# Optimization experiments

Measured on AMD Instinct MI355X. Metric: run time of the kernel, lower is better.

Reference implementation:

```python
import jax, jax.numpy as jnp
import numpy as np

RMS_EPS = 1e-6
B, S, H = 2, 4096, 4096
N_Q_OUT, N_KV_OUT = 4096, 1024  # 32 heads * 128, 8 kv heads * 128


def setup_inputs() -> dict:
    key = jax.random.key(0)
    k1, k2, k3, k4 = jax.random.split(key, 4)
    scale = 1.0 / np.sqrt(H)
    return {
        "hidden_states": jax.random.normal(k1, (B, S, H), dtype=jnp.float32),
        "gamma": jnp.ones((H,), dtype=jnp.float32),
        "w_q": jax.random.normal(k2, (H, N_Q_OUT), dtype=jnp.float32) * scale,
        "w_k": jax.random.normal(k3, (H, N_KV_OUT), dtype=jnp.float32) * scale,
        "w_v": jax.random.normal(k4, (H, N_KV_OUT), dtype=jnp.float32) * scale,
    }


def _rmsnorm(x, gamma, eps=RMS_EPS):
    # x: [B, S, H]; normalize over last axis
    var = jnp.mean(jnp.square(x), axis=-1, keepdims=True)
    return x * jax.lax.rsqrt(var + eps) * gamma


def reference(hidden_states, gamma, w_q, w_k, w_v):
    # Fused RMSNorm + QKV projection (GQA): normalize once, then three
    # column-parallel matmuls sharing the normalized activation.
    xn = _rmsnorm(hidden_states, gamma)  # [B, S, H]
    q = jnp.einsum("bsh,hd->bsd", xn, w_q)  # [B, S, n_heads*head_dim]
    k = jnp.einsum("bsh,hd->bsd", xn, w_k)  # [B, S, n_kv_heads*head_dim]
    v = jnp.einsum("bsh,hd->bsd", xn, w_v)  # [B, S, n_kv_heads*head_dim]
    return q, k, v
```

## Files before the change

### kernel.cpp

```cpp
#include <hip/hip_runtime.h>
#include <hip/hip_bf16.h>
#include <stdint.h>

#define HD      4096
#define MROWS   8192
#define NQ      4096
#define NKV     1024
#define NTOT    6144
#define RMS_EPS 1e-6f

typedef __attribute__((ext_vector_type(8))) short bf16x8;
typedef __attribute__((ext_vector_type(16))) float f32x16;

static __device__ __forceinline__ unsigned short f2bf(float f) {
  union { float f; unsigned u; } a; a.f = f;
  unsigned r = a.u + 0x7FFFu + ((a.u >> 16) & 1u);
  return (unsigned short)(r >> 16);
}

__global__ __launch_bounds__(256) void rmsnorm_cast_kernel(
    const float* __restrict__ x, const float* __restrict__ gamma,
    unsigned short* __restrict__ xn) {
  const int row = blockIdx.x;
  const float4* xr = (const float4*)(x + (size_t)row * HD);
  const float4* g4 = (const float4*)gamma;
  const int t = threadIdx.x;
  float4 v[4];
  float ss = 0.f;
#pragma unroll
  for (int i = 0; i < 4; ++i) {
    v[i] = xr[t + i * 256];
    ss += v[i].x * v[i].x + v[i].y * v[i].y + v[i].z * v[i].z + v[i].w * v[i].w;
  }
#pragma unroll
  for (int o = 32; o > 0; o >>= 1) ss += __shfl_xor(ss, o, 64);
  __shared__ float red[4];
  if ((t & 63) == 0) red[t >> 6] = ss;
  __syncthreads();
  const float tot = red[0] + red[1] + red[2] + red[3];
  const float rstd = rsqrtf(tot * (1.f / HD) + RMS_EPS);
  ushort4* xo = (ushort4*)(xn + (size_t)row * HD);
#pragma unroll
  for (int i = 0; i < 4; ++i) {
    const float4 g = g4[t + i * 256];
    ushort4 o;
    o.x = f2bf(v[i].x * rstd * g.x);
    o.y = f2bf(v[i].y * rstd * g.y);
    o.z = f2bf(v[i].z * rstd * g.z);
    o.w = f2bf(v[i].w * rstd * g.w);
    xo[t + i * 256] = o;
  }
}

__global__ __launch_bounds__(256) void transpose_cast_kernel(
    const float* __restrict__ w, unsigned short* __restrict__ wt, int Nw) {
  __shared__ float tile[32][33];
  const int kt = blockIdx.y;
  const int nb = blockIdx.x;
  const int t = threadIdx.x;
  const int r = t >> 3, c4 = t & 7;
  const float4 vin = *(const float4*)&w[(size_t)(kt * 32 + r) * Nw + nb * 32 + c4 * 4];
  tile[r][c4 * 4 + 0] = vin.x;
  tile[r][c4 * 4 + 1] = vin.y;
  tile[r][c4 * 4 + 2] = vin.z;
  tile[r][c4 * 4 + 3] = vin.w;
  __syncthreads();
  ushort4 o;
  o.x = f2bf(tile[c4 * 4 + 0][r]);
  o.y = f2bf(tile[c4 * 4 + 1][r]);
  o.z = f2bf(tile[c4 * 4 + 2][r]);
  o.w = f2bf(tile[c4 * 4 + 3][r]);
  *(ushort4*)&wt[(size_t)(nb * 32 + r) * HD + kt * 32 + c4 * 4] = o;
}


static __device__ __forceinline__ void gload_lds16(const unsigned short* g,
                                                   unsigned short* l) {
  __builtin_amdgcn_global_load_lds(
      (const __attribute__((address_space(1))) void*)g,
      (__attribute__((address_space(3))) void*)l, 16, 0, 0);
}

#define VM4 asm volatile("s_waitcnt vmcnt(4)" ::: "memory")
#define VM0 asm volatile("s_waitcnt vmcnt(0)" ::: "memory")

#define RD_A(BUF, HA)                                                          \
  do {                                                                         \
    const char* Ah = (const char*)&lds[0][BUF][HA][0];                         \
    _Pragma("unroll") for (int mi = 0; mi < 2; ++mi)                           \
      _Pragma("unroll") for (int ks = 0; ks < 4; ++ks)                         \
        af[mi][ks] = *(const bf16x8*)(Ah + (wr * 64 + mi * 32 + r32) * 128 +   \
                                      (((ks * 2 + hi) ^ swx) << 4));           \
  } while (0)

#define RD_B(BUF, HB)                                                          \
  do {                                                                         \
    const char* Bh = (const char*)&lds[1][BUF][HB][0];                         \
    _Pragma("unroll") for (int ks = 0; ks < 4; ++ks)                           \
      bfr[ks] = *(const bf16x8*)(Bh + (wc * 32 + r32) * 128 +                  \
                                 (((ks * 2 + hi) ^ swx) << 4));                \
  } while (0)

#define MMA(HA, HB)                                                            \
  do {                                                                         \
    __builtin_amdgcn_s_barrier();                                              \
    __builtin_amdgcn_s_setprio(1);                                             \
    _Pragma("unroll") for (int ks = 0; ks < 4; ++ks)                           \
      _Pragma("unroll") for (int mi = 0; mi < 2; ++mi)                         \
        acc[(HA) * 2 + mi][HB] = __builtin_amdgcn_mfma_f32_32x32x16_bf16(      \
            af[mi][ks], bfr[ks], acc[(HA) * 2 + mi][HB], 0, 0, 0);             \
    __builtin_amdgcn_s_setprio(0);                                             \
  } while (0)

__global__ __launch_bounds__(512, 2) void gemm_qkv_kernel(
    const unsigned short* __restrict__ A,
    const unsigned short* __restrict__ Bt,
    float* __restrict__ out) {
  __shared__ unsigned short lds[2][2][2][8192] __attribute__((aligned(16)));

  const int bid = blockIdx.x;
  const int xcd = bid & 7;
  const int idx = bid >> 3;
  const int sr  = idx >> 5;
  const int i32 = idx & 31;
  const int mt  = (xcd >> 1) * 8 + (i32 >> 2);
  const int nt  = (xcd & 1) * 12 + sr * 4 + (i32 & 3);
  const int m0 = mt * 256, n0 = nt * 256;

  const int tid = threadIdx.x;
  const int w = tid >> 6, lane = tid & 63;
  const int wr = w >> 2, wc = w & 3;
  const int r32 = lane & 31, hi = lane >> 5;
  const int swx = (r32 >> 1) & 7;

  const int wslot = w * 512;
  const int r3 = tid >> 3;
  const int scolb = (((tid & 7) ^ ((r3 >> 1) & 7))) << 4;
  const size_t so0 = (size_t)r3 * HD + (scolb >> 1);
  const size_t so1 = so0 + (size_t)64 * HD;

  const unsigned short* const Ab0 = A + (size_t)m0 * HD;
  const unsigned short* const Ab1 = Ab0 + (size_t)128 * HD;
  const unsigned short* const Bb0 = Bt + (size_t)n0 * HD;
  const unsigned short* const Bb1 = Bb0 + (size_t)128 * HD;

  auto STG = [&](const unsigned short* g, unsigned short* l) {
    gload_lds16(g + so0, l + wslot);
    gload_lds16(g + so1, l + 4096 + wslot);
  };

  f32x16 acc[4][2];
#pragma unroll
  for (int i = 0; i < 4; ++i)
#pragma unroll
    for (int j = 0; j < 2; ++j) acc[i][j] = (f32x16)(0.f);

  bf16x8 af[2][4];
  bf16x8 bfr[4];

  STG(Ab0, &lds[0][0][0][0]);
  STG(Bb0, &lds[1][0][0][0]);
  STG(Ab1, &lds[0][0][1][0]);
  STG(Bb1, &lds[1][0][1][0]);
  STG(Ab0 + 64, &lds[0][1][0][0]);
  STG(Bb0 + 64, &lds[1][1][0][0]);
  VM4;
  __builtin_amdgcn_s_barrier();

  for (int t = 0; t < 31; ++t) {
    const size_t k1 = (size_t)(2 * t + 1) * 64;
    const size_t o2 = (size_t)(2 * t + 2) * 64;
    const size_t o3 = (size_t)(2 * t + 3) * 64;
    RD_A(0, 0); RD_B(0, 1); STG(Ab1 + k1, &lds[0][1][1][0]);      MMA(0, 1);
    RD_B(0, 0);             STG(Bb1 + k1, &lds[1][1][1][0]);      MMA(0, 0);
    RD_A(0, 1);             STG(Ab0 + o2, &lds[0][0][0][0]);      MMA(1, 0);
    RD_B(0, 1);             STG(Bb0 + o2, &lds[1][0][0][0]); VM4; MMA(1, 1);
    RD_A(1, 0); RD_B(1, 1); STG(Ab1 + o2, &lds[0][0][1][0]);      MMA(0, 1);
    RD_B(1, 0);             STG(Bb1 + o2, &lds[1][0][1][0]);      MMA(0, 0);
    RD_A(1, 1);             STG(Ab0 + o3, &lds[0][1][0][0]);      MMA(1, 0);
    RD_B(1, 1);             STG(Bb0 + o3, &lds[1][1][0][0]); VM4; MMA(1, 1);
  }
  {
    const size_t k1 = (size_t)63 * 64;
    RD_A(0, 0); RD_B(0, 1); STG(Ab1 + k1, &lds[0][1][1][0]);      MMA(0, 1);
    RD_B(0, 0);             STG(Bb1 + k1, &lds[1][1][1][0]);      MMA(0, 0);
    RD_A(0, 1);                                                   MMA(1, 0);
    RD_B(0, 1);                                              VM0; MMA(1, 1);
    RD_A(1, 0); RD_B(1, 1);                                       MMA(0, 1);
    RD_B(1, 0);                                                   MMA(0, 0);
    RD_A(1, 1);                                                   MMA(1, 0);
    RD_B(1, 1);                                                   MMA(1, 1);
  }

  size_t obase; int ldc, nc;
  if (n0 < NQ)            { obase = 0;                                        ldc = NQ;  nc = n0; }
  else if (n0 < NQ + NKV) { obase = (size_t)MROWS * NQ;                       ldc = NKV; nc = n0 - NQ; }
  else                    { obase = (size_t)MROWS * NQ + (size_t)MROWS * NKV; ldc = NKV; nc = n0 - NQ - NKV; }

#pragma unroll
  for (int I = 0; I < 4; ++I) {
    const int rbase = m0 + (I >> 1) * 128 + wr * 64 + (I & 1) * 32 + hi * 4;
#pragma unroll
    for (int J = 0; J < 2; ++J) {
      const int col = nc + J * 128 + wc * 32 + r32;
#pragma unroll
      for (int reg = 0; reg < 16; ++reg) {
        const int row = rbase + (reg & 3) + 8 * (reg >> 2);
        out[obase + (size_t)row * ldc + col] = acc[I][J][reg];
      }
    }
  }
}

extern "C" void kernel_launch(void* const* d_in, const int* in_sizes, int n_in,
                              void* d_out, int out_size, void* d_ws, size_t ws_size,
                              hipStream_t stream) {
  const float* x     = (const float*)d_in[0];
  const float* gamma = (const float*)d_in[1];
  const float* wq    = (const float*)d_in[2];
  const float* wk    = (const float*)d_in[3];
  const float* wv    = (const float*)d_in[4];
  float* out = (float*)d_out;

  unsigned short* xn = (unsigned short*)d_ws;
  unsigned short* wt = xn + (size_t)MROWS * HD;

  rmsnorm_cast_kernel<<<MROWS, 256, 0, stream>>>(x, gamma, xn);
  transpose_cast_kernel<<<dim3(NQ / 32, HD / 32), 256, 0, stream>>>(wq, wt, NQ);
  transpose_cast_kernel<<<dim3(NKV / 32, HD / 32), 256, 0, stream>>>(
      wk, wt + (size_t)NQ * HD, NKV);
  transpose_cast_kernel<<<dim3(NKV / 32, HD / 32), 256, 0, stream>>>(
      wv, wt + (size_t)(NQ + NKV) * HD, NKV);
  gemm_qkv_kernel<<<(MROWS / 256) * (NTOT / 256), 512, 0, stream>>>(xn, wt, out);
}
```

Baseline: 416.0 us.

## Software-pipeline LDS fragment reads across MFMA halves with split K-subtiles

Splits each 64-wide K fragment into two halves with separate register sets, so LDS reads for the next MFMA group are issued while the current half's MFMAs run. Barriers move to after the MFMAs, and the global-to-LDS staging order is reshuffled with one extra prologue load and a deeper vmcnt wait. The goal is to hide LDS read latency behind matrix-core work. In exchange it needs more careful hazard ordering and may raise register pressure.

```diff
diff --git a/kernel.cpp b/kernel.cpp
--- a/kernel.cpp
+++ b/kernel.cpp
@@ -82,33 +82,57 @@
 }
 
 #define VM4 asm volatile("s_waitcnt vmcnt(4)" ::: "memory")
+#define VM6 asm volatile("s_waitcnt vmcnt(6)" ::: "memory")
 #define VM0 asm volatile("s_waitcnt vmcnt(0)" ::: "memory")
-
-#define RD_A(BUF, HA)                                                          \
+#define BAR __builtin_amdgcn_s_barrier()
+
+#define RA0(BUF, HA)                                                           \
   do {                                                                         \
     const char* Ah = (const char*)&lds[0][BUF][HA][0];                         \
     _Pragma("unroll") for (int mi = 0; mi < 2; ++mi)                           \
-      _Pragma("unroll") for (int ks = 0; ks < 4; ++ks)                         \
-        af[mi][ks] = *(const bf16x8*)(Ah + (wr * 64 + mi * 32 + r32) * 128 +   \
-                                      (((ks * 2 + hi) ^ swx) << 4));           \
-  } while (0)
-
-#define RD_B(BUF, HB)                                                          \
+      _Pragma("unroll") for (int k = 0; k < 2; ++k)                            \
+        af0[mi][k] = *(const bf16x8*)(Ah + (wr * 64 + mi * 32 + r32) * 128 +   \
+                                      (((k * 2 + hi) ^ swx) << 4));            \
+  } while (0)
+#define RA1(BUF, HA)                                                           \
+  do {                                                                         \
+    const char* Ah = (const char*)&lds[0][BUF][HA][0];                         \
+    _Pragma("unroll") for (int mi = 0; mi < 2; ++mi)                           \
+      _Pragma("unroll") for (int k = 0; k < 2; ++k)                            \
+        af1[mi][k] = *(const bf16x8*)(Ah + (wr * 64 + mi * 32 + r32) * 128 +   \
+                                      ((((k + 2) * 2 + hi) ^ swx) << 4));      \
+  } while (0)
+#define RB0(BUF, HB)                                                           \
   do {                                                                         \
     const char* Bh = (const char*)&lds[1][BUF][HB][0];                         \
-    _Pragma("unroll") for (int ks = 0; ks < 4; ++ks)                           \
-      bfr[ks] = *(const bf16x8*)(Bh + (wc * 32 + r32) * 128 +                  \
-                                 (((ks * 2 + hi) ^ swx) << 4));                \
-  } while (0)
-
-#define MMA(HA, HB)                                                            \
-  do {                                                                         \
-    __builtin_amdgcn_s_barrier();                                              \
+    _Pragma("unroll") for (int k = 0; k < 2; ++k)                              \
+      bf0[k] = *(const bf16x8*)(Bh + (wc * 32 + r32) * 128 +                   \
+                                (((k * 2 + hi) ^ swx) << 4));                  \
+  } while (0)
+#define RB1(BUF, HB)                                                           \
+  do {                                                                         \
+    const char* Bh = (const char*)&lds[1][BUF][HB][0];                         \
+    _Pragma("unroll") for (int k = 0; k < 2; ++k)                              \
+      bf1[k] = *(const bf16x8*)(Bh + (wc * 32 + r32) * 128 +                   \
+                                ((((k + 2) * 2 + hi) ^ swx) << 4));            \
+  } while (0)
+
+#define M0(HA, HB)                                                             \
+  do {                                                                         \
     __builtin_amdgcn_s_setprio(1);                                             \
-    _Pragma("unroll") for (int ks = 0; ks < 4; ++ks)                           \
+    _Pragma("unroll") for (int k = 0; k < 2; ++k)                              \
       _Pragma("unroll") for (int mi = 0; mi < 2; ++mi)                         \
         acc[(HA) * 2 + mi][HB] = __builtin_amdgcn_mfma_f32_32x32x16_bf16(      \
-            af[mi][ks], bfr[ks], acc[(HA) * 2 + mi][HB], 0, 0, 0);             \
+            af0[mi][k], bf0[k], acc[(HA) * 2 + mi][HB], 0, 0, 0);              \
+    __builtin_amdgcn_s_setprio(0);                                             \
+  } while (0)
+#define M1(HA, HB)                                                             \
+  do {                                                                         \
+    __builtin_amdgcn_s_setprio(1);                                             \
+    _Pragma("unroll") for (int k = 0; k < 2; ++k)                              \
+      _Pragma("unroll") for (int mi = 0; mi < 2; ++mi)                         \
+        acc[(HA) * 2 + mi][HB] = __builtin_amdgcn_mfma_f32_32x32x16_bf16(      \
+            af1[mi][k], bf1[k], acc[(HA) * 2 + mi][HB], 0, 0, 0);              \
     __builtin_amdgcn_s_setprio(0);                                             \
   } while (0)
 
@@ -155,41 +179,52 @@
 #pragma unroll
     for (int j = 0; j < 2; ++j) acc[i][j] = (f32x16)(0.f);
 
-  bf16x8 af[2][4];
-  bf16x8 bfr[4];
-
-  STG(Ab0, &lds[0][0][0][0]);
-  STG(Bb0, &lds[1][0][0][0]);
-  STG(Ab1, &lds[0][0][1][0]);
-  STG(Bb1, &lds[1][0][1][0]);
+  bf16x8 af0[2][2], af1[2][2];
+  bf16x8 bf0[2], bf1[2];
+
+  STG(Ab0,      &lds[0][0][0][0]);
+  STG(Bb1,      &lds[1][0][1][0]);
+  STG(Ab1,      &lds[0][0][1][0]);
+  STG(Bb0,      &lds[1][0][0][0]);
   STG(Ab0 + 64, &lds[0][1][0][0]);
   STG(Bb0 + 64, &lds[1][1][0][0]);
-  VM4;
-  __builtin_amdgcn_s_barrier();
+  STG(Ab1 + 64, &lds[0][1][1][0]);
+  VM6;
+  BAR;
+  RA0(0, 0); RB0(0, 1);
 
   for (int t = 0; t < 31; ++t) {
     const size_t k1 = (size_t)(2 * t + 1) * 64;
     const size_t o2 = (size_t)(2 * t + 2) * 64;
     const size_t o3 = (size_t)(2 * t + 3) * 64;
-    RD_A(0, 0); RD_B(0, 1); STG(Ab1 + k1, &lds[0][1][1][0]);      MMA(0, 1);
-    RD_B(0, 0);             STG(Bb1 + k1, &lds[1][1][1][0]);      MMA(0, 0);
-    RD_A(0, 1);             STG(Ab0 + o2, &lds[0][0][0][0]);      MMA(1, 0);
-    RD_B(0, 1);             STG(Bb0 + o2, &lds[1][0][0][0]); VM4; MMA(1, 1);
-    RD_A(1, 0); RD_B(1, 1); STG(Ab1 + o2, &lds[0][0][1][0]);      MMA(0, 1);
-    RD_B(1, 0);             STG(Bb1 + o2, &lds[1][0][1][0]);      MMA(0, 0);
-    RD_A(1, 1);             STG(Ab0 + o3, &lds[0][1][0][0]);      MMA(1, 0);
-    RD_B(1, 1);             STG(Bb0 + o3, &lds[1][1][0][0]); VM4; MMA(1, 1);
+    RA1(0, 0); RB1(0, 1); STG(Bb1 + k1, &lds[1][1][1][0]);
+    M0(0, 1); RB0(0, 0); M1(0, 1); BAR;
+    RB1(0, 0); STG(Ab0 + o2, &lds[0][0][0][0]);
+    M0(0, 0); RA0(0, 1); M1(0, 0); BAR;
+    RA1(0, 1); STG(Bb0 + o2, &lds[1][0][0][0]);
+    M0(1, 0); RB0(0, 1); M1(1, 0); VM4; BAR;
+    RB1(0, 1); STG(Ab1 + o2, &lds[0][0][1][0]);
+    M0(1, 1); RA0(1, 0); RB0(1, 1); M1(1, 1); BAR;
+    RA1(1, 0); RB1(1, 1); STG(Bb1 + o2, &lds[1][0][1][0]);
+    M0(0, 1); RB0(1, 0); M1(0, 1); BAR;
+    RB1(1, 0); STG(Ab0 + o3, &lds[0][1][0][0]);
+    M0(0, 0); RA0(1, 1); M1(0, 0); BAR;
+    RA1(1, 1); STG(Bb0 + o3, &lds[1][1][0][0]);
+    M0(1, 0); RB0(1, 1); M1(1, 0); VM4; BAR;
+    RB1(1, 1); STG(Ab1 + o3, &lds[0][1][1][0]);
+    M0(1, 1); RA0(0, 0); RB0(0, 1); M1(1, 1); BAR;
   }
   {
     const size_t k1 = (size_t)63 * 64;
-    RD_A(0, 0); RD_B(0, 1); STG(Ab1 + k1, &lds[0][1][1][0]);      MMA(0, 1);
-    RD_B(0, 0);             STG(Bb1 + k1, &lds[1][1][1][0]);      MMA(0, 0);
-    RD_A(0, 1);                                                   MMA(1, 0);
-    RD_B(0, 1);                                              VM0; MMA(1, 1);
-    RD_A(1, 0); RD_B(1, 1);                                       MMA(0, 1);
-    RD_B(1, 0);                                                   MMA(0, 0);
-    RD_A(1, 1);                                                   MMA(1, 0);
-    RD_B(1, 1);                                                   MMA(1, 1);
+    RA1(0, 0); RB1(0, 1); STG(Bb1 + k1, &lds[1][1][1][0]);
+    M0(0, 1); RB0(0, 0); M1(0, 1); BAR;
+    RB1(0, 0); M0(0, 0); RA0(0, 1); M1(0, 0); BAR;
+    RA1(0, 1); M0(1, 0); RB0(0, 1); M1(1, 0); VM0; BAR;
+    RB1(0, 1); M0(1, 1); RA0(1, 0); RB0(1, 1); M1(1, 1); BAR;
+    RA1(1, 0); RB1(1, 1); M0(0, 1); RB0(1, 0); M1(0, 1); BAR;
+    RB1(1, 0); M0(0, 0); RA0(1, 1); M1(0, 0); BAR;
+    RA1(1, 1); M0(1, 0); RB0(1, 1); M1(1, 0); BAR;
+    RB1(1, 1); M0(1, 1); M1(1, 1);
   }
 
   size_t obase; int ldc, nc;
```

Measured after the change: 413.5 us. Within noise of the previous version (-0.6%).

## Restructure GEMM main loop with register double-buffering and deeper load prefetch

Applied to the files above, without the earlier changes.

Rewrites the GEMM K-loop so the A and B fragments are double-buffered in registers, which lets the LDS reads for the next sub-tile go out before the MFMAs of the current one run. Both 128-row halves of the next K-tile are prefetched up front, and the waitcnt thresholds are raised so more global-to-LDS loads stay in flight. The tail iterations are folded into the main loop by clamping the K offsets, so the last iterations issue redundant loads. The extra fragment registers raise VGPR pressure under the 512x2 launch bound, and the barrier placement changes in ways that could race.

```diff
diff --git a/kernel.cpp b/kernel.cpp
--- a/kernel.cpp
+++ b/kernel.cpp
@@ -81,35 +81,55 @@
       (__attribute__((address_space(3))) void*)l, 16, 0, 0);
 }
 
-#define VM4 asm volatile("s_waitcnt vmcnt(4)" ::: "memory")
+#define VM6 asm volatile("s_waitcnt vmcnt(6)" ::: "memory")
+#define VM8 asm volatile("s_waitcnt vmcnt(8)" ::: "memory")
 #define VM0 asm volatile("s_waitcnt vmcnt(0)" ::: "memory")
-
-#define RD_A(BUF, HA)                                                          \
+#define BAR __builtin_amdgcn_s_barrier()
+
+#define RD_A(DST, BUF, HA)                                                     \
   do {                                                                         \
     const char* Ah = (const char*)&lds[0][BUF][HA][0];                         \
     _Pragma("unroll") for (int mi = 0; mi < 2; ++mi)                           \
-      _Pragma("unroll") for (int ks = 0; ks < 4; ++ks)                         \
-        af[mi][ks] = *(const bf16x8*)(Ah + (wr * 64 + mi * 32 + r32) * 128 +   \
-                                      (((ks * 2 + hi) ^ swx) << 4));           \
-  } while (0)
-
-#define RD_B(BUF, HB)                                                          \
+      _Pragma("unroll") for (int k = 0; k < 4; ++k)                            \
+        DST[mi][k] = *(const bf16x8*)(Ah + (wr * 64 + mi * 32 + r32) * 128 +   \
+                                      (((k * 2 + hi) ^ swx) << 4));            \
+  } while (0)
+
+#define RD_B(DST, BUF, HB)                                                     \
   do {                                                                         \
     const char* Bh = (const char*)&lds[1][BUF][HB][0];                         \
-    _Pragma("unroll") for (int ks = 0; ks < 4; ++ks)                           \
-      bfr[ks] = *(const bf16x8*)(Bh + (wc * 32 + r32) * 128 +                  \
-                                 (((ks * 2 + hi) ^ swx) << 4));                \
-  } while (0)
-
-#define MMA(HA, HB)                                                            \
-  do {                                                                         \
-    __builtin_amdgcn_s_barrier();                                              \
+    _Pragma("unroll") for (int k = 0; k < 4; ++k)                              \
+      DST[k] = *(const bf16x8*)(Bh + (wc * 32 + r32) * 128 +                   \
+                                (((k * 2 + hi) ^ swx) << 4));                  \
+  } while (0)
+
+#define MM8(I0, I1, J, AR, BR)                                                 \
+  do {                                                                         \
     __builtin_amdgcn_s_setprio(1);                                             \
-    _Pragma("unroll") for (int ks = 0; ks < 4; ++ks)                           \
-      _Pragma("unroll") for (int mi = 0; mi < 2; ++mi)                         \
-        acc[(HA) * 2 + mi][HB] = __builtin_amdgcn_mfma_f32_32x32x16_bf16(      \
-            af[mi][ks], bfr[ks], acc[(HA) * 2 + mi][HB], 0, 0, 0);             \
+    _Pragma("unroll") for (int k = 0; k < 4; ++k) {                            \
+      acc[I0][J] = __builtin_amdgcn_mfma_f32_32x32x16_bf16(                    \
+          AR[0][k], BR[k], acc[I0][J], 0, 0, 0);                               \
+      acc[I1][J] = __builtin_amdgcn_mfma_f32_32x32x16_bf16(                    \
+          AR[1][k], BR[k], acc[I1][J], 0, 0, 0);                               \
+    }                                                                          \
     __builtin_amdgcn_s_setprio(0);                                             \
+  } while (0)
+
+#define TILE(BUF, NBUF, BB, NB, KO)                                            \
+  do {                                                                         \
+                                                                       \
+    VM6; RD_A(a1, BUF, 1); STG(Ab0 + (KO), &lds[0][BUF][0][0]); BAR;           \
+    MM8(0, 1, 0, a0, b0r[BB]);                                                 \
+                                                                       \
+    STG(Bb0 + (KO), &lds[1][BUF][0][0]); BAR;                                  \
+    MM8(0, 1, 1, a0, b1r);                                                     \
+                                                                       \
+    VM6; RD_A(a0, NBUF, 0); STG(Bb1 + (KO), &lds[1][BUF][1][0]); BAR;          \
+    MM8(2, 3, 1, a1, b1r);                                                     \
+                                                                       \
+    RD_B(b1r, NBUF, 1); RD_B(b0r[NB], NBUF, 0);                                \
+    STG(Ab1 + (KO), &lds[0][BUF][1][0]); BAR;                                  \
+    MM8(2, 3, 0, a1, b0r[BB]);                                                 \
   } while (0)
 
 __global__ __launch_bounds__(512, 2) void gemm_qkv_kernel(
@@ -155,42 +175,30 @@
 #pragma unroll
     for (int j = 0; j < 2; ++j) acc[i][j] = (f32x16)(0.f);
 
-  bf16x8 af[2][4];
-  bf16x8 bfr[4];
-
-  STG(Ab0, &lds[0][0][0][0]);
-  STG(Bb0, &lds[1][0][0][0]);
-  STG(Ab1, &lds[0][0][1][0]);
-  STG(Bb1, &lds[1][0][1][0]);
+  bf16x8 a0[2][4], a1[2][4];
+  bf16x8 b1r[4];
+  bf16x8 b0r[2][4];
+
+  STG(Ab0,      &lds[0][0][0][0]);
+  STG(Bb0,      &lds[1][0][0][0]);
+  STG(Bb1,      &lds[1][0][1][0]);
+  STG(Ab1,      &lds[0][0][1][0]);
   STG(Ab0 + 64, &lds[0][1][0][0]);
   STG(Bb0 + 64, &lds[1][1][0][0]);
-  VM4;
-  __builtin_amdgcn_s_barrier();
-
-  for (int t = 0; t < 31; ++t) {
-    const size_t k1 = (size_t)(2 * t + 1) * 64;
-    const size_t o2 = (size_t)(2 * t + 2) * 64;
-    const size_t o3 = (size_t)(2 * t + 3) * 64;
-    RD_A(0, 0); RD_B(0, 1); STG(Ab1 + k1, &lds[0][1][1][0]);      MMA(0, 1);
-    RD_B(0, 0);             STG(Bb1 + k1, &lds[1][1][1][0]);      MMA(0, 0);
-    RD_A(0, 1);             STG(Ab0 + o2, &lds[0][0][0][0]);      MMA(1, 0);
-    RD_B(0, 1);             STG(Bb0 + o2, &lds[1][0][0][0]); VM4; MMA(1, 1);
-    RD_A(1, 0); RD_B(1, 1); STG(Ab1 + o2, &lds[0][0][1][0]);      MMA(0, 1);
-    RD_B(1, 0);             STG(Bb1 + o2, &lds[1][0][1][0]);      MMA(0, 0);
-    RD_A(1, 1);             STG(Ab0 + o3, &lds[0][1][0][0]);      MMA(1, 0);
-    RD_B(1, 1);             STG(Bb0 + o3, &lds[1][1][0][0]); VM4; MMA(1, 1);
-  }
-  {
-    const size_t k1 = (size_t)63 * 64;
-    RD_A(0, 0); RD_B(0, 1); STG(Ab1 + k1, &lds[0][1][1][0]);      MMA(0, 1);
-    RD_B(0, 0);             STG(Bb1 + k1, &lds[1][1][1][0]);      MMA(0, 0);
-    RD_A(0, 1);                                                   MMA(1, 0);
-    RD_B(0, 1);                                              VM0; MMA(1, 1);
-    RD_A(1, 0); RD_B(1, 1);                                       MMA(0, 1);
-    RD_B(1, 0);                                                   MMA(0, 0);
-    RD_A(1, 1);                                                   MMA(1, 0);
-    RD_B(1, 1);                                                   MMA(1, 1);
-  }
+  STG(Bb1 + 64, &lds[1][1][1][0]);
+  STG(Ab1 + 64, &lds[0][1][1][0]);
+  VM8;
+  BAR;
+  RD_A(a0, 0, 0); RD_B(b0r[0], 0, 0); RD_B(b1r, 0, 1);
+
+  for (int t = 0; t < 32; ++t) {
+    const int t2 = 2 * t + 2, t3 = 2 * t + 3;
+    const size_t ko2 = (size_t)(t2 < 64 ? t2 : 63) * 64;
+    const size_t ko3 = (size_t)(t3 < 64 ? t3 : 63) * 64;
+    TILE(0, 1, 0, 1, ko2);
+    TILE(1, 0, 1, 0, ko3);
+  }
+  VM0;
 
   size_t obase; int ldc, nc;
   if (n0 < NQ)            { obase = 0;                                        ldc = NQ;  nc = n0; }
```

Result: slower. 1.565 ms (+276.3%).

## Merge prep kernels and restructure GEMM main loop warp tiling and barriers

Applied to the files above, without the earlier changes.

The rmsnorm and the three weight transpose-cast kernels are merged into one launch with a block-index dispatch, removing three launches and the tail gaps between them. The GEMM reassigns each warp to a 128x64 output subtile, precomputes the LDS read pointers, and reorders the staging so B tiles are loaded ahead of A. It also puts barriers on both sides of every MFMA group and clamps the final prefetches so one uniform 32-iteration loop replaces the peeled epilogue. The extra barriers may add synchronisation stalls, and the clamped last iterations issue redundant loads.

```diff
diff --git a/kernel.cpp b/kernel.cpp
--- a/kernel.cpp
+++ b/kernel.cpp
@@ -18,59 +18,61 @@
   return (unsigned short)(r >> 16);
 }
 
-__global__ __launch_bounds__(256) void rmsnorm_cast_kernel(
+__global__ __launch_bounds__(256) void prep_kernel(
     const float* __restrict__ x, const float* __restrict__ gamma,
-    unsigned short* __restrict__ xn) {
-  const int row = blockIdx.x;
-  const float4* xr = (const float4*)(x + (size_t)row * HD);
-  const float4* g4 = (const float4*)gamma;
+    const float* __restrict__ wq, const float* __restrict__ wk,
+    const float* __restrict__ wv,
+    unsigned short* __restrict__ xn, unsigned short* __restrict__ wt) {
+  __shared__ float smem[32 * 33];
+  const int bid = blockIdx.x;
   const int t = threadIdx.x;
-  float4 v[4];
-  float ss = 0.f;
-#pragma unroll
-  for (int i = 0; i < 4; ++i) {
-    v[i] = xr[t + i * 256];
-    ss += v[i].x * v[i].x + v[i].y * v[i].y + v[i].z * v[i].z + v[i].w * v[i].w;
-  }
-#pragma unroll
-  for (int o = 32; o > 0; o >>= 1) ss += __shfl_xor(ss, o, 64);
-  __shared__ float red[4];
-  if ((t & 63) == 0) red[t >> 6] = ss;
-  __syncthreads();
-  const float tot = red[0] + red[1] + red[2] + red[3];
-  const float rstd = rsqrtf(tot * (1.f / HD) + RMS_EPS);
-  ushort4* xo = (ushort4*)(xn + (size_t)row * HD);
-#pragma unroll
-  for (int i = 0; i < 4; ++i) {
-    const float4 g = g4[t + i * 256];
+  if (bid < MROWS) {
+    const float4* xr = (const float4*)(x + (size_t)bid * HD);
+    const float4* g4 = (const float4*)gamma;
+    float4 v[4];
+    float ss = 0.f;
+#pragma unroll
+    for (int i = 0; i < 4; ++i) {
+      v[i] = xr[t + i * 256];
+      ss += v[i].x * v[i].x + v[i].y * v[i].y + v[i].z * v[i].z + v[i].w * v[i].w;
+    }
+#pragma unroll
+    for (int o = 32; o > 0; o >>= 1) ss += __shfl_xor(ss, o, 64);
+    if ((t & 63) == 0) smem[t >> 6] = ss;
+    __syncthreads();
+    const float tot = smem[0] + smem[1] + smem[2] + smem[3];
+    const float rstd = rsqrtf(tot * (1.f / HD) + RMS_EPS);
+    ushort4* xo = (ushort4*)(xn + (size_t)bid * HD);
+#pragma unroll
+    for (int i = 0; i < 4; ++i) {
+      const float4 g = g4[t + i * 256];
+      ushort4 o;
+      o.x = f2bf(v[i].x * rstd * g.x);
+      o.y = f2bf(v[i].y * rstd * g.y);
+      o.z = f2bf(v[i].z * rstd * g.z);
+      o.w = f2bf(v[i].w * rstd * g.w);
+      xo[t + i * 256] = o;
+    }
+  } else {
+    int b2 = bid - MROWS;
+    const float* w; unsigned short* dst; int Nw, nb, kt;
+    if (b2 < 16384)      { w = wq; dst = wt;                           Nw = NQ;  nb = b2 & 127; kt = b2 >> 7; }
+    else if (b2 < 20480) { b2 -= 16384; w = wk; dst = wt + (size_t)NQ * HD;         Nw = NKV; nb = b2 & 31; kt = b2 >> 5; }
+    else                 { b2 -= 20480; w = wv; dst = wt + (size_t)(NQ + NKV) * HD; Nw = NKV; nb = b2 & 31; kt = b2 >> 5; }
+    const int r = t >> 3, c4 = t & 7;
+    const float4 vin = *(const float4*)&w[(size_t)(kt * 32 + r) * Nw + nb * 32 + c4 * 4];
+    smem[r * 33 + c4 * 4 + 0] = vin.x;
+    smem[r * 33 + c4 * 4 + 1] = vin.y;
+    smem[r * 33 + c4 * 4 + 2] = vin.z;
+    smem[r * 33 + c4 * 4 + 3] = vin.w;
+    __syncthreads();
     ushort4 o;
-    o.x = f2bf(v[i].x * rstd * g.x);
-    o.y = f2bf(v[i].y * rstd * g.y);
-    o.z = f2bf(v[i].z * rstd * g.z);
-    o.w = f2bf(v[i].w * rstd * g.w);
-    xo[t + i * 256] = o;
-  }
-}
-
-__global__ __launch_bounds__(256) void transpose_cast_kernel(
-    const float* __restrict__ w, unsigned short* __restrict__ wt, int Nw) {
-  __shared__ float tile[32][33];
-  const int kt = blockIdx.y;
-  const int nb = blockIdx.x;
-  const int t = threadIdx.x;
-  const int r = t >> 3, c4 = t & 7;
-  const float4 vin = *(const float4*)&w[(size_t)(kt * 32 + r) * Nw + nb * 32 + c4 * 4];
-  tile[r][c4 * 4 + 0] = vin.x;
-  tile[r][c4 * 4 + 1] = vin.y;
-  tile[r][c4 * 4 + 2] = vin.z;
-  tile[r][c4 * 4 + 3] = vin.w;
-  __syncthreads();
-  ushort4 o;
-  o.x = f2bf(tile[c4 * 4 + 0][r]);
-  o.y = f2bf(tile[c4 * 4 + 1][r]);
-  o.z = f2bf(tile[c4 * 4 + 2][r]);
-  o.w = f2bf(tile[c4 * 4 + 3][r]);
-  *(ushort4*)&wt[(size_t)(nb * 32 + r) * HD + kt * 32 + c4 * 4] = o;
+    o.x = f2bf(smem[(c4 * 4 + 0) * 33 + r]);
+    o.y = f2bf(smem[(c4 * 4 + 1) * 33 + r]);
+    o.z = f2bf(smem[(c4 * 4 + 2) * 33 + r]);
+    o.w = f2bf(smem[(c4 * 4 + 3) * 33 + r]);
+    *(ushort4*)&dst[(size_t)(nb * 32 + r) * HD + kt * 32 + c4 * 4] = o;
+  }
 }
 
 
@@ -83,32 +85,28 @@
 
 #define VM4 asm volatile("s_waitcnt vmcnt(4)" ::: "memory")
 #define VM0 asm volatile("s_waitcnt vmcnt(0)" ::: "memory")
-
-#define RD_A(BUF, HA)                                                          \
+#define BAR __builtin_amdgcn_s_barrier()
+
+#define RDA(AK, QM)                                                            \
   do {                                                                         \
-    const char* Ah = (const char*)&lds[0][BUF][HA][0];                         \
     _Pragma("unroll") for (int mi = 0; mi < 2; ++mi)                           \
       _Pragma("unroll") for (int ks = 0; ks < 4; ++ks)                         \
-        af[mi][ks] = *(const bf16x8*)(Ah + (wr * 64 + mi * 32 + r32) * 128 +   \
-                                      (((ks * 2 + hi) ^ swx) << 4));           \
+        ar[mi][ks] = *(const bf16x8*)(AK[ks] + (QM) * 8192 + mi * 4096);       \
   } while (0)
 
-#define RD_B(BUF, HB)                                                          \
+#define RDB(DST, BK, QN)                                                       \
   do {                                                                         \
-    const char* Bh = (const char*)&lds[1][BUF][HB][0];                         \
     _Pragma("unroll") for (int ks = 0; ks < 4; ++ks)                           \
-      bfr[ks] = *(const bf16x8*)(Bh + (wc * 32 + r32) * 128 +                  \
-                                 (((ks * 2 + hi) ^ swx) << 4));                \
+      DST[ks] = *(const bf16x8*)(BK[ks] + (QN) * 4096);                        \
   } while (0)
 
-#define MMA(HA, HB)                                                            \
+#define MMA8(QM, QN, BR)                                                       \
   do {                                                                         \
-    __builtin_amdgcn_s_barrier();                                              \
     __builtin_amdgcn_s_setprio(1);                                             \
     _Pragma("unroll") for (int ks = 0; ks < 4; ++ks)                           \
       _Pragma("unroll") for (int mi = 0; mi < 2; ++mi)                         \
-        acc[(HA) * 2 + mi][HB] = __builtin_amdgcn_mfma_f32_32x32x16_bf16(      \
-            af[mi][ks], bfr[ks], acc[(HA) * 2 + mi][HB], 0, 0, 0);             \
+        acc[(QM) * 2 + mi][QN] = __builtin_amdgcn_mfma_f32_32x32x16_bf16(      \
+            ar[mi][ks], BR[ks], acc[(QM) * 2 + mi][QN], 0, 0, 0);              \
     __builtin_amdgcn_s_setprio(0);                                             \
   } while (0)
 
@@ -133,11 +131,23 @@
   const int r32 = lane & 31, hi = lane >> 5;
   const int swx = (r32 >> 1) & 7;
 
+  const int rowoff = r32 * 128;
+  const char* a0k[4]; const char* a1k[4];
+  const char* b0k[4]; const char* b1k[4];
+#pragma unroll
+  for (int ks = 0; ks < 4; ++ks) {
+    const int sl = (((ks * 2 + hi) ^ swx) << 4);
+    a0k[ks] = (const char*)&lds[0][0][wr][0] + rowoff + sl;
+    a1k[ks] = (const char*)&lds[0][1][wr][0] + rowoff + sl;
+    b0k[ks] = (const char*)&lds[1][0][wc >> 1][0] + (wc & 1) * 8192 + rowoff + sl;
+    b1k[ks] = (const char*)&lds[1][1][wc >> 1][0] + (wc & 1) * 8192 + rowoff + sl;
+  }
+
   const int wslot = w * 512;
   const int r3 = tid >> 3;
-  const int scolb = (((tid & 7) ^ ((r3 >> 1) & 7))) << 4;
-  const size_t so0 = (size_t)r3 * HD + (scolb >> 1);
-  const size_t so1 = so0 + (size_t)64 * HD;
+  const unsigned scol = (unsigned)(((tid & 7) ^ ((r3 >> 1) & 7)) << 3);
+  const unsigned so0 = (unsigned)r3 * HD + scol;
+  const unsigned so1 = so0 + 64u * HD;
 
   const unsigned short* const Ab0 = A + (size_t)m0 * HD;
   const unsigned short* const Ab1 = Ab0 + (size_t)128 * HD;
@@ -155,42 +165,41 @@
 #pragma unroll
     for (int j = 0; j < 2; ++j) acc[i][j] = (f32x16)(0.f);
 
-  bf16x8 af[2][4];
-  bf16x8 bfr[4];
-
-  STG(Ab0, &lds[0][0][0][0]);
-  STG(Bb0, &lds[1][0][0][0]);
-  STG(Ab1, &lds[0][0][1][0]);
-  STG(Bb1, &lds[1][0][1][0]);
-  STG(Ab0 + 64, &lds[0][1][0][0]);
+  bf16x8 ar[2][4];
+  bf16x8 br0[4], br1[4];
+
+  STG(Bb0,      &lds[1][0][0][0]);
+  STG(Bb1,      &lds[1][0][1][0]);
+  STG(Ab0,      &lds[0][0][0][0]);
+  STG(Ab1,      &lds[0][0][1][0]);
   STG(Bb0 + 64, &lds[1][1][0][0]);
+  STG(Bb1 + 64, &lds[1][1][1][0]);
   VM4;
-  __builtin_amdgcn_s_barrier();
-
-  for (int t = 0; t < 31; ++t) {
-    const size_t k1 = (size_t)(2 * t + 1) * 64;
-    const size_t o2 = (size_t)(2 * t + 2) * 64;
-    const size_t o3 = (size_t)(2 * t + 3) * 64;
-    RD_A(0, 0); RD_B(0, 1); STG(Ab1 + k1, &lds[0][1][1][0]);      MMA(0, 1);
-    RD_B(0, 0);             STG(Bb1 + k1, &lds[1][1][1][0]);      MMA(0, 0);
-    RD_A(0, 1);             STG(Ab0 + o2, &lds[0][0][0][0]);      MMA(1, 0);
-    RD_B(0, 1);             STG(Bb0 + o2, &lds[1][0][0][0]); VM4; MMA(1, 1);
-    RD_A(1, 0); RD_B(1, 1); STG(Ab1 + o2, &lds[0][0][1][0]);      MMA(0, 1);
-    RD_B(1, 0);             STG(Bb1 + o2, &lds[1][0][1][0]);      MMA(0, 0);
-    RD_A(1, 1);             STG(Ab0 + o3, &lds[0][1][0][0]);      MMA(1, 0);
-    RD_B(1, 1);             STG(Bb0 + o3, &lds[1][1][0][0]); VM4; MMA(1, 1);
-  }
-  {
-    const size_t k1 = (size_t)63 * 64;
-    RD_A(0, 0); RD_B(0, 1); STG(Ab1 + k1, &lds[0][1][1][0]);      MMA(0, 1);
-    RD_B(0, 0);             STG(Bb1 + k1, &lds[1][1][1][0]);      MMA(0, 0);
-    RD_A(0, 1);                                                   MMA(1, 0);
-    RD_B(0, 1);                                              VM0; MMA(1, 1);
-    RD_A(1, 0); RD_B(1, 1);                                       MMA(0, 1);
-    RD_B(1, 0);                                                   MMA(0, 0);
-    RD_A(1, 1);                                                   MMA(1, 0);
-    RD_B(1, 1);                                                   MMA(1, 1);
-  }
+  BAR;
+
+  for (int t = 0; t < 32; ++t) {
+    const int kcs = (2 * t + 1) * 64;
+    const int t2 = 2 * t + 2, t3 = 2 * t + 3;
+    const int kc0 = (t2 < 64 ? t2 : 63) * 64;
+    const int kc1 = (t3 < 64 ? t3 : 63) * 64;
+    RDA(a0k, 0); RDB(br0, b0k, 0); STG(Ab0 + kcs, &lds[0][1][0][0]);
+    BAR; MMA8(0, 0, br0); BAR;
+    RDB(br1, b0k, 1);              STG(Ab1 + kcs, &lds[0][1][1][0]);
+    BAR; MMA8(0, 1, br1); BAR;
+    RDA(a0k, 1);                   STG(Bb0 + kc0, &lds[1][0][0][0]);
+    BAR; MMA8(1, 0, br0); BAR;
+                                   STG(Bb1 + kc0, &lds[1][0][1][0]); VM4;
+    BAR; MMA8(1, 1, br1); BAR;
+    RDA(a1k, 0); RDB(br0, b1k, 0); STG(Ab0 + kc0, &lds[0][0][0][0]);
+    BAR; MMA8(0, 0, br0); BAR;
+    RDB(br1, b1k, 1);              STG(Ab1 + kc0, &lds[0][0][1][0]);
+    BAR; MMA8(0, 1, br1); BAR;
+    RDA(a1k, 1);                   STG(Bb0 + kc1, &lds[1][1][0][0]);
+    BAR; MMA8(1, 0, br0); BAR;
+                                   STG(Bb1 + kc1, &lds[1][1][1][0]); VM4;
+    BAR; MMA8(1, 1, br1); BAR;
+  }
+  VM0;
 
   size_t obase; int ldc, nc;
   if (n0 < NQ)            { obase = 0;                                        ldc = NQ;  nc = n0; }
@@ -199,10 +208,10 @@
 
 #pragma unroll
   for (int I = 0; I < 4; ++I) {
-    const int rbase = m0 + (I >> 1) * 128 + wr * 64 + (I & 1) * 32 + hi * 4;
+    const int rbase = m0 + wr * 128 + I * 32 + hi * 4;
 #pragma unroll
     for (int J = 0; J < 2; ++J) {
-      const int col = nc + J * 128 + wc * 32 + r32;
+      const int col = nc + wc * 64 + J * 32 + r32;
 #pragma unroll
       for (int reg = 0; reg < 16; ++reg) {
         const int row = rbase + (reg & 3) + 8 * (reg >> 2);
@@ -225,11 +234,6 @@
   unsigned short* xn = (unsigned short*)d_ws;
   unsigned short* wt = xn + (size_t)MROWS * HD;
 
-  rmsnorm_cast_kernel<<<MROWS, 256, 0, stream>>>(x, gamma, xn);
-  transpose_cast_kernel<<<dim3(NQ / 32, HD / 32), 256, 0, stream>>>(wq, wt, NQ);
-  transpose_cast_kernel<<<dim3(NKV / 32, HD / 32), 256, 0, stream>>>(
-      wk, wt + (size_t)NQ * HD, NKV);
-  transpose_cast_kernel<<<dim3(NKV / 32, HD / 32), 256, 0, stream>>>(
-      wv, wt + (size_t)(NQ + NKV) * HD, NKV);
+  prep_kernel<<<32768, 256, 0, stream>>>(x, gamma, wq, wk, wv, xn, wt);
   gemm_qkv_kernel<<<(MROWS / 256) * (NTOT / 256), 512, 0, stream>>>(xn, wt, out);
 }
```

New measurement: 422.3 us. About the same (+1.5%).
